# Performance work log

Hardware: AMD Instinct MI355X
Metric: run time of the kernel (lower is better)

The kernel has to match this reference:

```python
import jax, jax.numpy as jnp
import numpy as np


def _rot_grids(group_order, ks, dtype):
    """Normalized sampling grids for each rotation (align_corners=False convention)."""
    k = jnp.arange(group_order, dtype=dtype)
    theta = 2.0 * jnp.pi * k / group_order                      # [G]
    c, s = jnp.cos(theta), jnp.sin(theta)
    # F.affine_grid base coords with align_corners=False: centers of pixels in [-1,1]
    lin = (jnp.arange(ks, dtype=dtype) + 0.5) * (2.0 / ks) - 1.0
    y, x = jnp.meshgrid(lin, lin, indexing='ij')                 # [ks,ks] each
    # theta rows: [cos, -sin, 0], [sin, cos, 0] applied to (x, y, 1)
    gx = c[:, None, None] * x - s[:, None, None] * y             # [G,ks,ks]
    gy = s[:, None, None] * x + c[:, None, None] * y             # [G,ks,ks]
    return gx, gy


def _grid_sample_bilinear_zeros(img, gx, gy):
    """Bilinear grid_sample, padding_mode='zeros', align_corners=False.
    img: [C,H,W]; gx,gy: [G,H,W] normalized coords. Returns [C,G,H,W]."""
    C, H, W = img.shape
    dt = img.dtype
    # unnormalize (align_corners=False)
    ix = ((gx + 1.0) * W - 1.0) * 0.5
    iy = ((gy + 1.0) * H - 1.0) * 0.5
    ix0 = jnp.floor(ix)
    iy0 = jnp.floor(iy)
    wx1 = (ix - ix0).astype(dt); wx0 = 1.0 - wx1
    wy1 = (iy - iy0).astype(dt); wy0 = 1.0 - wy1

    def gather(iyf, ixf):
        xi = ixf.astype(jnp.int32)
        yi = iyf.astype(jnp.int32)
        valid = ((xi >= 0) & (xi < W) & (yi >= 0) & (yi < H)).astype(dt)
        xi_c = jnp.clip(xi, 0, W - 1)
        yi_c = jnp.clip(yi, 0, H - 1)
        return img[:, yi_c, xi_c] * valid                        # [C,G,H,W]

    out = (gather(iy0, ix0) * (wy0 * wx0)
           + gather(iy0, ix0 + 1.0) * (wy0 * wx1)
           + gather(iy0 + 1.0, ix0) * (wy1 * wx0)
           + gather(iy0 + 1.0, ix0 + 1.0) * (wy1 * wx1))
    return out


def setup_inputs() -> dict:
    key = jax.random.key(0)
    out_ch, in_ch, ks = 512, 256, 9
    base_weight = jax.random.normal(key, (out_ch, in_ch, ks, ks), dtype=jnp.float32)
    return {"base_weight": base_weight, "group_order": 8}


def reference(base_weight, group_order):
    O, I, ks, _ = base_weight.shape
    img = base_weight.reshape(O * I, ks, ks)                     # [C,H,W]
    gx, gy = _rot_grids(group_order, ks, base_weight.dtype)      # [G,ks,ks]
    out = _grid_sample_bilinear_zeros(img, gx, gy)               # [C,G,ks,ks]
    # concat over rotations along dim 0 -> [G*O, I, ks, ks]
    out = out.reshape(O, I, group_order, ks, ks).transpose(2, 0, 1, 3, 4)
    return out.reshape(group_order * O, I, ks, ks)
```

## Files before the change

kernel.cpp:

```cpp
#include <hip/hip_runtime.h>
#include <math.h>


#define KS   9
#define NPIX 81
#define NC   128
#define BLOCK 256

__global__ void st_make_table(float* __restrict__ tab, int G) {
    int i = blockIdx.x * blockDim.x + threadIdx.x;
    if (i >= G * NPIX) return;
    int g = i / NPIX;
    int p = i - g * NPIX;
    int py = p / KS, px = p - py * KS;
    double theta = 6.283185307179586 * (double)g / (double)G;
    double cth = cos(theta), sth = sin(theta);
    double lx = ((double)px + 0.5) * (2.0 / KS) - 1.0;
    double ly = ((double)py + 0.5) * (2.0 / KS) - 1.0;
    double gx = cth * lx - sth * ly;
    double gy = sth * lx + cth * ly;
    double ix = ((gx + 1.0) * KS - 1.0) * 0.5;
    double iy = ((gy + 1.0) * KS - 1.0) * 0.5;
    double ix0 = floor(ix), iy0 = floor(iy);
    double fx = ix - ix0, fy = iy - iy0;
    int xi0 = (int)ix0, yi0 = (int)iy0;
    float w[4]; int o[4];
#pragma unroll
    for (int k = 0; k < 4; ++k) {
        int dx = k & 1, dy = k >> 1;
        int xi = xi0 + dx, yi = yi0 + dy;
        bool valid = (xi >= 0) && (xi < KS) && (yi >= 0) && (yi < KS);
        double wv = (dy ? fy : 1.0 - fy) * (dx ? fx : 1.0 - fx);
        int xc = xi < 0 ? 0 : (xi > KS - 1 ? KS - 1 : xi);
        int yc = yi < 0 ? 0 : (yi > KS - 1 ? KS - 1 : yi);
        w[k] = valid ? (float)wv : 0.0f;
        o[k] = (yc * KS + xc) * 4;
    }
    float4* e0 = (float4*)(tab + (size_t)i * 8);
    *e0 = make_float4(w[0], w[1], w[2], w[3]);
    int4* e1 = (int4*)(tab + (size_t)i * 8 + 4);
    *e1 = make_int4(o[0], o[1], o[2], o[3]);
}

__global__ __launch_bounds__(BLOCK) void st_rotate(
        const float* __restrict__ in, const float* __restrict__ tab,
        float* __restrict__ out, int C, int G) {
    __shared__ __align__(16) float lin[NC * NPIX];
    const int t = threadIdx.x;
    const int c0 = blockIdx.x * NC;

    {
        const float4* src = (const float4*)(in + (size_t)c0 * NPIX);
        float4* dst = (float4*)lin;
        for (int j = t; j < NC * NPIX / 4; j += BLOCK) dst[j] = src[j];
    }
    __syncthreads();

    if (t < 3 * NPIX) {
        const int c_local = t / NPIX;
        const int p = t - c_local * NPIX;
        const float4* tab4 = (const float4*)tab;
        for (int g = 0; g < G; ++g) {
            const float4 w = tab4[(size_t)(g * NPIX + p) * 2];
            const int4  o = ((const int4*)tab4)[(size_t)(g * NPIX + p) * 2 + 1];
            float* og = out + ((size_t)g * C + c0) * NPIX + t;
            const char* lb = (const char*)lin + c_local * (NPIX * 4);
            for (int cc = 0; cc < NC; cc += 3) {
                if (cc + c_local < NC) {
                    float v = *(const float*)(lb + o.x) * w.x
                            + *(const float*)(lb + o.y) * w.y
                            + *(const float*)(lb + o.z) * w.z
                            + *(const float*)(lb + o.w) * w.w;
                    *og = v;
                }
                lb += 3 * NPIX * 4;
                og += 3 * NPIX;
            }
        }
    }
}

extern "C" void kernel_launch(void* const* d_in, const int* in_sizes, int n_in,
                              void* d_out, int out_size, void* d_ws, size_t ws_size,
                              hipStream_t stream) {
    const float* in = (const float*)d_in[0];
    float* out = (float*)d_out;
    float* tab = (float*)d_ws;
    const int C = in_sizes[0] / NPIX;
    const int G = out_size / in_sizes[0];
    const int ents = G * NPIX;
    st_make_table<<<(ents + 255) / 256, 256, 0, stream>>>(tab, G);
    st_rotate<<<C / NC, BLOCK, 0, stream>>>(in, tab, out, C, G);
}
```

Baseline: 384.0 us.

## Halve channels per block, compact table to row-pair offsets, prefetch next rotation

```diff
diff --git a/kernel.cpp b/kernel.cpp
--- a/kernel.cpp
+++ b/kernel.cpp
@@ -4,7 +4,7 @@
 
 #define KS   9
 #define NPIX 81
-#define NC   128
+#define NC   64
 #define BLOCK 256
 
 __global__ void st_make_table(float* __restrict__ tab, int G) {
@@ -23,26 +23,31 @@
     double iy = ((gy + 1.0) * KS - 1.0) * 0.5;
     double ix0 = floor(ix), iy0 = floor(iy);
     double fx = ix - ix0, fy = iy - iy0;
-    int xi0 = (int)ix0, yi0 = (int)iy0;
-    float w[4]; int o[4];
-#pragma unroll
-    for (int k = 0; k < 4; ++k) {
-        int dx = k & 1, dy = k >> 1;
-        int xi = xi0 + dx, yi = yi0 + dy;
-        bool valid = (xi >= 0) && (xi < KS) && (yi >= 0) && (yi < KS);
-        double wv = (dy ? fy : 1.0 - fy) * (dx ? fx : 1.0 - fx);
-        int xc = xi < 0 ? 0 : (xi > KS - 1 ? KS - 1 : xi);
-        int yc = yi < 0 ? 0 : (yi > KS - 1 ? KS - 1 : yi);
-        w[k] = valid ? (float)wv : 0.0f;
-        o[k] = (yc * KS + xc) * 4;
-    }
+    int x0 = (int)ix0, y0 = (int)iy0;
+
+    double wx0 = 1.0 - fx, wx1 = fx;
+    double pw0, pw1; int xs;
+    if (x0 >= 0 && x0 < KS - 1)      { xs = x0;     pw0 = wx0; pw1 = wx1; }
+    else if (x0 == KS - 1)           { xs = KS - 2; pw0 = 0.0; pw1 = wx0; }
+    else if (x0 == -1)               { xs = 0;      pw0 = wx1; pw1 = 0.0; }
+    else                             { xs = 0;      pw0 = 0.0; pw1 = 0.0; }
+
+    int yA = y0, yB = y0 + 1;
+    double wyA = (yA >= 0 && yA < KS) ? (1.0 - fy) : 0.0;
+    double wyB = (yB >= 0 && yB < KS) ? fy : 0.0;
+    int yAc = yA < 0 ? 0 : (yA > KS - 1 ? KS - 1 : yA);
+    int yBc = yB < 0 ? 0 : (yB > KS - 1 ? KS - 1 : yB);
+    int offA = (yAc * KS + xs) * 4;
+    int offB = (yBc * KS + xs) * 4;
+
     float4* e0 = (float4*)(tab + (size_t)i * 8);
-    *e0 = make_float4(w[0], w[1], w[2], w[3]);
+    *e0 = make_float4((float)(wyA * pw0), (float)(wyA * pw1),
+                      (float)(wyB * pw0), (float)(wyB * pw1));
     int4* e1 = (int4*)(tab + (size_t)i * 8 + 4);
-    *e1 = make_int4(o[0], o[1], o[2], o[3]);
+    *e1 = make_int4(offA, offB, 0, 0);
 }
 
-__global__ __launch_bounds__(BLOCK) void st_rotate(
+__global__ __launch_bounds__(BLOCK, 8) void st_rotate(
         const float* __restrict__ in, const float* __restrict__ tab,
         float* __restrict__ out, int C, int G) {
     __shared__ __align__(16) float lin[NC * NPIX];
@@ -52,31 +57,49 @@
     {
         const float4* src = (const float4*)(in + (size_t)c0 * NPIX);
         float4* dst = (float4*)lin;
-        for (int j = t; j < NC * NPIX / 4; j += BLOCK) dst[j] = src[j];
+#pragma unroll
+        for (int j = 0; j < (NC * NPIX / 4 + BLOCK - 1) / BLOCK; ++j) {
+            int idx = t + j * BLOCK;
+            if (idx < NC * NPIX / 4) dst[idx] = src[idx];
+        }
     }
     __syncthreads();
 
-    if (t < 3 * NPIX) {
-        const int c_local = t / NPIX;
-        const int p = t - c_local * NPIX;
-        const float4* tab4 = (const float4*)tab;
-        for (int g = 0; g < G; ++g) {
-            const float4 w = tab4[(size_t)(g * NPIX + p) * 2];
-            const int4  o = ((const int4*)tab4)[(size_t)(g * NPIX + p) * 2 + 1];
-            float* og = out + ((size_t)g * C + c0) * NPIX + t;
-            const char* lb = (const char*)lin + c_local * (NPIX * 4);
-            for (int cc = 0; cc < NC; cc += 3) {
-                if (cc + c_local < NC) {
-                    float v = *(const float*)(lb + o.x) * w.x
-                            + *(const float*)(lb + o.y) * w.y
-                            + *(const float*)(lb + o.z) * w.z
-                            + *(const float*)(lb + o.w) * w.w;
-                    *og = v;
-                }
-                lb += 3 * NPIX * 4;
-                og += 3 * NPIX;
-            }
+    if (t >= 3 * NPIX) return;
+    const int c_local = t / NPIX;
+    const int p = t - c_local * NPIX;
+    const float4* tw = (const float4*)tab;
+    const int4* ti = (const int4*)tab;
+
+    float4 w = tw[(size_t)p * 2];
+    int4  ob = ti[(size_t)p * 2 + 1];
+
+    for (int g = 0; g < G; ++g) {
+        float4 wn; int4 obn;
+        if (g + 1 < G) {
+            wn  = tw[(size_t)((g + 1) * NPIX + p) * 2];
+            obn = ti[(size_t)((g + 1) * NPIX + p) * 2 + 1];
         }
+        const char* lb = (const char*)lin + c_local * (NPIX * 4);
+        float* og = out + ((size_t)g * C + c0) * NPIX + t;
+#pragma unroll 3
+        for (int k = 0; k < NC / 3; ++k) {
+            float a0 = *(const float*)(lb + ob.x);
+            float a1 = *(const float*)(lb + ob.x + 4);
+            float b0 = *(const float*)(lb + ob.y);
+            float b1 = *(const float*)(lb + ob.y + 4);
+            *og = a0 * w.x + a1 * w.y + b0 * w.z + b1 * w.w;
+            lb += 3 * NPIX * 4;
+            og += 3 * NPIX;
+        }
+        if (c_local == 0) {
+            float a0 = *(const float*)(lb + ob.x);
+            float a1 = *(const float*)(lb + ob.x + 4);
+            float b0 = *(const float*)(lb + ob.y);
+            float b1 = *(const float*)(lb + ob.y + 4);
+            *og = a0 * w.x + a1 * w.y + b0 * w.z + b1 * w.w;
+        }
+        w = wn; ob = obn;
     }
 }
 
```

New measurement: 387.2 us. No clear change (+0.8%).
